# Kernel tuning notes

Measured on AMD Instinct MI355X. Metric: run time of the kernel, lower is better.

The kernel has to match this reference:

```python
import jax, jax.numpy as jnp
import numpy as np
import math

B, S, D, NPOS = 8, 2048, 768, 512


def setup_inputs() -> dict:
    key = jax.random.key(0)
    ks = jax.random.split(key, 9)
    std = 0.02
    return {
        "token_embeddings": jax.random.normal(ks[0], (B, S, D), dtype=jnp.float32),
        "attention_mask": jnp.ones((B, S), dtype=jnp.int32),
        "Wq": jax.random.normal(ks[1], (D, D), dtype=jnp.float32) * std,
        "bq": jax.random.normal(ks[2], (D,), dtype=jnp.float32) * std,
        "Wk": jax.random.normal(ks[3], (D, D), dtype=jnp.float32) * std,
        "bk": jax.random.normal(ks[4], (D,), dtype=jnp.float32) * std,
        "Wv": jax.random.normal(ks[5], (D, D), dtype=jnp.float32) * std,
        "bv": jax.random.normal(ks[6], (D,), dtype=jnp.float32) * std,
        "pos_emb": jax.random.normal(ks[7], (D, NPOS), dtype=jnp.float32) * std,
    }


def reference(token_embeddings, attention_mask, Wq, bq, Wk, bk, Wv, bv, pos_emb):
    scale = 1.0 / math.sqrt(D)
    q = token_embeddings @ Wq.T + bq  # [B,S,D]
    k = token_embeddings @ Wk.T + bk
    v = token_embeddings @ Wv.T + bv

    logits = jnp.einsum("bsd,btd->bst", q, k) * scale  # [B,S,S]
    logits = jnp.where(attention_mask[:, None, :] == 0, -jnp.inf, logits)

    # CoPE: gate-based fractional positions + interpolated learned bias
    gates = jax.nn.sigmoid(logits)
    pos = jnp.flip(jnp.cumsum(jnp.flip(gates, -1), axis=-1), -1)  # reverse cumsum
    pos = jnp.minimum(pos, float(NPOS - 1))
    pos_floor = jnp.floor(pos)
    pos_ceil = jnp.ceil(pos)
    logits_int = jnp.einsum("bsd,dn->bsn", q, pos_emb)  # [B,S,NPOS]
    lc = jnp.take_along_axis(logits_int, pos_ceil.astype(jnp.int32), axis=-1)
    lf = jnp.take_along_axis(logits_int, pos_floor.astype(jnp.int32), axis=-1)
    w = pos - pos_floor
    logits = logits + lc * w + lf * (1.0 - w)

    attn = jax.nn.softmax(logits, axis=-1)
    out = jnp.einsum("bst,btd->bsd", attn, v)
    return out[:, 0, :]  # CLS pooled sentence embedding [B,D]
```

## Files before the change

### kernel.cpp

```cpp
#include <hip/hip_runtime.h>
#include <hip/hip_bf16.h>
#include <math.h>

#define BB 8
#define SS 2048
#define DD 768
#define NPOS 512
#define TC 64
#define DSPLIT 16
#define DCHUNK (DD / DSPLIT)
#define ETOT 1280
#define SCALE 0.036084391824351615f

#define WS_Q      0
#define WS_QK     6144
#define WS_LI     12288
#define WS_LOGITS 16384
#define WS_ATTN   32768
#define WS_CTX    49152
#define WS_PART   55296
#define WS_PWS    448512

__device__ __forceinline__ float wave_reduce_sum(float v) {
    #pragma unroll
    for (int off = 32; off > 0; off >>= 1) v += __shfl_xor(v, off, 64);
    return v;
}

__global__ __launch_bounds__(256) void k_gemv(const float* __restrict__ vecs, size_t vstride,
        const float* __restrict__ W, const float* __restrict__ bias,
        float* __restrict__ out) {
    int gw = (blockIdx.x * 256 + threadIdx.x) >> 6;
    int lane = threadIdx.x & 63;
    if (gw >= BB * DD) return;
    int b = gw / DD, d = gw % DD;
    const float4* vr = (const float4*)(vecs + (size_t)b * vstride);
    const float4* wr = (const float4*)(W + (size_t)d * DD);
    float acc = 0.f;
    #pragma unroll
    for (int j = 0; j < 3; ++j) {
        float4 a = vr[lane + 64 * j];
        float4 w = wr[lane + 64 * j];
        acc += a.x * w.x + a.y * w.y + a.z * w.z + a.w * w.w;
    }
    acc = wave_reduce_sum(acc);
    if (lane == 0) out[gw] = acc + bias[d];
}

__global__ __launch_bounds__(256) void k_qkw(const float* __restrict__ q,
        const float* __restrict__ Wk, const float* __restrict__ pos_emb,
        float* __restrict__ pws) {
    int part = blockIdx.x, ds = blockIdx.y, tid = threadIdx.x;
    __shared__ float qs[BB][DCHUNK];
    for (int i = tid; i < BB * DCHUNK; i += 256) {
        int b = i / DCHUNK, d = i % DCHUNK;
        qs[b][d] = q[b * DD + ds * DCHUNK + d];
    }
    __syncthreads();
    const float* Wsrc; int stride, eg;
    if (part < 3) { Wsrc = Wk; stride = DD; eg = part * 256 + tid; }
    else { Wsrc = pos_emb; stride = NPOS; eg = DD + (part - 3) * 256 + tid; }
    int e = (part < 3) ? eg : eg - DD;
    const float* col = Wsrc + (size_t)(ds * DCHUNK) * stride + e;
    float acc[BB];
    #pragma unroll
    for (int b = 0; b < BB; ++b) acc[b] = 0.f;
    #pragma unroll
    for (int d = 0; d < DCHUNK; ++d) {
        float w = col[(size_t)d * stride];
        #pragma unroll
        for (int b = 0; b < BB; ++b) acc[b] += qs[b][d] * w;
    }
    #pragma unroll
    for (int b = 0; b < BB; ++b)
        pws[((size_t)ds * BB + b) * ETOT + eg] = acc[b];
}

__global__ __launch_bounds__(256) void k_qkr(const float* __restrict__ pws,
        float* __restrict__ qk, float* __restrict__ lint) {
    int idx = blockIdx.x * 256 + threadIdx.x;
    if (idx >= BB * ETOT) return;
    int b = idx / ETOT, e = idx % ETOT;
    float acc = 0.f;
    #pragma unroll
    for (int ds = 0; ds < DSPLIT; ++ds)
        acc += pws[((size_t)ds * BB + b) * ETOT + e];
    if (e < DD) qk[b * DD + e] = acc;
    else lint[b * NPOS + (e - DD)] = acc;
}

__global__ __launch_bounds__(256) void k_logits(const float* __restrict__ x,
        const float* __restrict__ qk, const float* __restrict__ q,
        const float* __restrict__ bk,
        const int* __restrict__ mask, float* __restrict__ logits) {
    int gw = (blockIdx.x * 256 + threadIdx.x) >> 6;
    int lane = threadIdx.x & 63;
    if (gw >= BB * SS) return;
    int b = gw / SS;
    const float4* xr = (const float4*)(x + (size_t)gw * DD);
    const float4* wr = (const float4*)(qk + (size_t)b * DD);
    const float4* qr = (const float4*)(q + (size_t)b * DD);
    const float4* br = (const float4*)bk;
    float acc = 0.f;
    #pragma unroll
    for (int j = 0; j < 3; ++j) {
        float4 a = xr[lane + 64 * j];
        float4 w = wr[lane + 64 * j];
        acc += a.x * w.x + a.y * w.y + a.z * w.z + a.w * w.w;
        float4 qv = qr[lane + 64 * j];
        float4 bv = br[lane + 64 * j];
        acc += qv.x * bv.x + qv.y * bv.y + qv.z * bv.z + qv.w * bv.w;
    }
    acc = wave_reduce_sum(acc);
    if (lane == 0) {
        float lg = acc * SCALE;
        logits[gw] = mask[gw] ? lg : -INFINITY;
    }
}

__global__ __launch_bounds__(256) void k_scan(const float* __restrict__ logits,
        const float* __restrict__ lint, float* __restrict__ attn) {
    int b = blockIdx.x, tid = threadIdx.x;
    __shared__ float lg[SS];
    __shared__ float li[NPOS];
    __shared__ float sa[256], sb[256];
    for (int i = tid; i < SS; i += 256) lg[i] = logits[b * SS + i];
    for (int i = tid; i < NPOS; i += 256) li[i] = lint[b * NPOS + i];
    __syncthreads();
    int base = tid * 8;
    float loc[8];
    float run = 0.f;
    #pragma unroll
    for (int k = 7; k >= 0; --k) {
        float v = lg[base + k];
        float gk = 1.f / (1.f + expf(-v));
        run += gk;
        loc[k] = run;
    }
    sa[tid] = run;
    __syncthreads();
    float* src = sa; float* dst = sb;
    for (int off = 1; off < 256; off <<= 1) {
        float v = src[tid];
        if (tid + off < 256) v += src[tid + off];
        dst[tid] = v;
        __syncthreads();
        float* t_ = src; src = dst; dst = t_;
    }
    float st = (tid < 255) ? src[tid + 1] : 0.f;
    float adj[8];
    float m = -INFINITY;
    #pragma unroll
    for (int k = 0; k < 8; ++k) {
        float v = lg[base + k];
        float nv;
        if (v == -INFINITY) {
            nv = v;
        } else {
            float p = fminf(loc[k] + st, (float)(NPOS - 1));
            float pf = floorf(p);
            float w = p - pf;
            int fi = (int)pf;
            int ci = (int)ceilf(p);
            nv = v + li[ci] * w + li[fi] * (1.f - w);
        }
        adj[k] = nv;
        m = fmaxf(m, nv);
    }
    __syncthreads();
    sa[tid] = m;
    __syncthreads();
    for (int s2 = 128; s2 > 0; s2 >>= 1) {
        if (tid < s2) sa[tid] = fmaxf(sa[tid], sa[tid + s2]);
        __syncthreads();
    }
    float bm = sa[0];
    __syncthreads();
    float sum = 0.f;
    #pragma unroll
    for (int k = 0; k < 8; ++k) { adj[k] = expf(adj[k] - bm); sum += adj[k]; }
    sa[tid] = sum;
    __syncthreads();
    for (int s2 = 128; s2 > 0; s2 >>= 1) {
        if (tid < s2) sa[tid] += sa[tid + s2];
        __syncthreads();
    }
    float inv = 1.f / sa[0];
    float4* out4 = (float4*)(attn + b * SS + base);
    out4[0] = make_float4(adj[0] * inv, adj[1] * inv, adj[2] * inv, adj[3] * inv);
    out4[1] = make_float4(adj[4] * inv, adj[5] * inv, adj[6] * inv, adj[7] * inv);
}

__global__ __launch_bounds__(192) void k_ctx_part(const float* __restrict__ x,
        const float* __restrict__ attn, float* __restrict__ part) {
    int tc = blockIdx.x, b = blockIdx.y, tid = threadIdx.x;
    const int TPC = SS / TC;
    float4 acc = make_float4(0.f, 0.f, 0.f, 0.f);
    const float4* xr = (const float4*)(x + ((size_t)b * SS + (size_t)tc * TPC) * DD);
    const float* at = attn + b * SS + tc * TPC;
    for (int i = 0; i < TPC; ++i) {
        float a = at[i];
        float4 xv = xr[(size_t)i * 192 + tid];
        acc.x += a * xv.x; acc.y += a * xv.y; acc.z += a * xv.z; acc.w += a * xv.w;
    }
    ((float4*)(part + (size_t)(b * TC + tc) * DD))[tid] = acc;
}

__global__ __launch_bounds__(256) void k_ctx_red(const float* __restrict__ part,
        float* __restrict__ ctx) {
    int idx = blockIdx.x * 256 + threadIdx.x;
    if (idx >= BB * DD) return;
    int b = idx / DD, e = idx % DD;
    float acc = 0.f;
    #pragma unroll 4
    for (int tc = 0; tc < TC; ++tc) acc += part[(size_t)(b * TC + tc) * DD + e];
    ctx[idx] = acc;
}

extern "C" void kernel_launch(void* const* d_in, const int* in_sizes, int n_in,
                              void* d_out, int out_size, void* d_ws, size_t ws_size,
                              hipStream_t stream) {
    const float* x       = (const float*)d_in[0];
    const int*   mask    = (const int*)  d_in[1];
    const float* Wq      = (const float*)d_in[2];
    const float* bq      = (const float*)d_in[3];
    const float* Wk      = (const float*)d_in[4];
    const float* bk      = (const float*)d_in[5];
    const float* Wv      = (const float*)d_in[6];
    const float* bv      = (const float*)d_in[7];
    const float* pos_emb = (const float*)d_in[8];
    float* out = (float*)d_out;

    float* ws     = (float*)d_ws;
    float* q      = ws + WS_Q;
    float* qk     = ws + WS_QK;
    float* lint   = ws + WS_LI;
    float* logits = ws + WS_LOGITS;
    float* attn   = ws + WS_ATTN;
    float* ctx    = ws + WS_CTX;
    float* part   = ws + WS_PART;
    float* pws    = ws + WS_PWS;

    k_gemv<<<dim3((BB * DD) / 4), dim3(256), 0, stream>>>(x, (size_t)SS * DD, Wq, bq, q);
    k_qkw<<<dim3(5, DSPLIT), dim3(256), 0, stream>>>(q, Wk, pos_emb, pws);
    k_qkr<<<dim3((BB * ETOT + 255) / 256), dim3(256), 0, stream>>>(pws, qk, lint);
    k_logits<<<dim3((BB * SS) / 4), dim3(256), 0, stream>>>(x, qk, q, bk, mask, logits);
    k_scan<<<dim3(BB), dim3(256), 0, stream>>>(logits, lint, attn);
    k_ctx_part<<<dim3(TC, BB), dim3(192), 0, stream>>>(x, attn, part);
    k_ctx_red<<<dim3((BB * DD + 255) / 256), dim3(256), 0, stream>>>(part, ctx);
    k_gemv<<<dim3((BB * DD) / 4), dim3(256), 0, stream>>>(ctx, (size_t)DD, Wv, bv, out);
}
```

Baseline: 49.80 us.

## Replace split-reduction kernels with atomics and use wave shuffles in scan

Removes the two separate reduction kernels (for q·Wk/pos_emb partials and the context partials) by accumulating with atomicAdd into zeroed buffers, cutting the launch count from eight to six. The zeroing is folded into the Q kernel and the scan kernel. The q·bk term is precomputed once per batch instead of being recomputed by every logit wave. The scan kernel's suffix sum, max and sum reductions now use wave shuffles with far fewer barriers. Atomics make the floating-point summation order nondeterministic, and DSPLIT doubles, which raises atomic traffic.

New measurement: 46.38 us. 6.9% less time.

```diff
diff --git a/kernel.cpp b/kernel.cpp
--- a/kernel.cpp
+++ b/kernel.cpp
@@ -7,35 +7,40 @@
 #define DD 768
 #define NPOS 512
 #define TC 64
-#define DSPLIT 16
+#define DSPLIT 32
 #define DCHUNK (DD / DSPLIT)
-#define ETOT 1280
 #define SCALE 0.036084391824351615f
 
 #define WS_Q      0
 #define WS_QK     6144
 #define WS_LI     12288
-#define WS_LOGITS 16384
-#define WS_ATTN   32768
-#define WS_CTX    49152
-#define WS_PART   55296
-#define WS_PWS    448512
-
-__device__ __forceinline__ float wave_reduce_sum(float v) {
+#define WS_QBK    16384
+#define WS_LOGITS 16400
+#define WS_ATTN   32784
+#define WS_CTX    49168
+
+__device__ __forceinline__ float wave_sum(float v) {
     #pragma unroll
     for (int off = 32; off > 0; off >>= 1) v += __shfl_xor(v, off, 64);
     return v;
 }
-
-__global__ __launch_bounds__(256) void k_gemv(const float* __restrict__ vecs, size_t vstride,
-        const float* __restrict__ W, const float* __restrict__ bias,
-        float* __restrict__ out) {
-    int gw = (blockIdx.x * 256 + threadIdx.x) >> 6;
+__device__ __forceinline__ float wave_max(float v) {
+    #pragma unroll
+    for (int off = 32; off > 0; off >>= 1) v = fmaxf(v, __shfl_xor(v, off, 64));
+    return v;
+}
+
+__global__ __launch_bounds__(256) void k_q(const float* __restrict__ x,
+        const float* __restrict__ Wq, const float* __restrict__ bq,
+        float* __restrict__ q, float* __restrict__ qkz) {
+    int zi = blockIdx.x * 256 + threadIdx.x;
+    if (zi < DD * BB + NPOS * BB) qkz[zi] = 0.f;
+    int gw = zi >> 6;
     int lane = threadIdx.x & 63;
     if (gw >= BB * DD) return;
     int b = gw / DD, d = gw % DD;
-    const float4* vr = (const float4*)(vecs + (size_t)b * vstride);
-    const float4* wr = (const float4*)(W + (size_t)d * DD);
+    const float4* vr = (const float4*)(x + (size_t)b * SS * DD);
+    const float4* wr = (const float4*)(Wq + (size_t)d * DD);
     float acc = 0.f;
     #pragma unroll
     for (int j = 0; j < 3; ++j) {
@@ -43,13 +48,14 @@
         float4 w = wr[lane + 64 * j];
         acc += a.x * w.x + a.y * w.y + a.z * w.z + a.w * w.w;
     }
-    acc = wave_reduce_sum(acc);
-    if (lane == 0) out[gw] = acc + bias[d];
+    acc = wave_sum(acc);
+    if (lane == 0) q[gw] = acc + bq[d];
 }
 
 __global__ __launch_bounds__(256) void k_qkw(const float* __restrict__ q,
         const float* __restrict__ Wk, const float* __restrict__ pos_emb,
-        float* __restrict__ pws) {
+        const float* __restrict__ bk,
+        float* __restrict__ qk, float* __restrict__ lint, float* __restrict__ qbk) {
     int part = blockIdx.x, ds = blockIdx.y, tid = threadIdx.x;
     __shared__ float qs[BB][DCHUNK];
     for (int i = tid; i < BB * DCHUNK; i += 256) {
@@ -57,10 +63,10 @@
         qs[b][d] = q[b * DD + ds * DCHUNK + d];
     }
     __syncthreads();
-    const float* Wsrc; int stride, eg;
-    if (part < 3) { Wsrc = Wk; stride = DD; eg = part * 256 + tid; }
-    else { Wsrc = pos_emb; stride = NPOS; eg = DD + (part - 3) * 256 + tid; }
-    int e = (part < 3) ? eg : eg - DD;
+    const float* Wsrc; int stride; float* dst; int e;
+    if (part < 3) { Wsrc = Wk; stride = DD; dst = qk; e = part * 256 + tid; }
+    else { Wsrc = pos_emb; stride = NPOS; dst = lint; e = (part - 3) * 256 + tid; }
+    int ncols = (part < 3) ? DD : NPOS;
     const float* col = Wsrc + (size_t)(ds * DCHUNK) * stride + e;
     float acc[BB];
     #pragma unroll
@@ -72,26 +78,24 @@
         for (int b = 0; b < BB; ++b) acc[b] += qs[b][d] * w;
     }
     #pragma unroll
-    for (int b = 0; b < BB; ++b)
-        pws[((size_t)ds * BB + b) * ETOT + eg] = acc[b];
-}
-
-__global__ __launch_bounds__(256) void k_qkr(const float* __restrict__ pws,
-        float* __restrict__ qk, float* __restrict__ lint) {
-    int idx = blockIdx.x * 256 + threadIdx.x;
-    if (idx >= BB * ETOT) return;
-    int b = idx / ETOT, e = idx % ETOT;
-    float acc = 0.f;
-    #pragma unroll
-    for (int ds = 0; ds < DSPLIT; ++ds)
-        acc += pws[((size_t)ds * BB + b) * ETOT + e];
-    if (e < DD) qk[b * DD + e] = acc;
-    else lint[b * NPOS + (e - DD)] = acc;
+    for (int b = 0; b < BB; ++b) atomicAdd(&dst[b * ncols + e], acc[b]);
+    if (part == 0 && ds == 0) {
+        int w = tid >> 6, lane = tid & 63;
+        #pragma unroll
+        for (int r = 0; r < 2; ++r) {
+            int b = w + 4 * r;
+            float p = 0.f;
+            #pragma unroll
+            for (int j = 0; j < 12; ++j)
+                p += q[b * DD + lane + 64 * j] * bk[lane + 64 * j];
+            p = wave_sum(p);
+            if (lane == 0) qbk[b] = p;
+        }
+    }
 }
 
 __global__ __launch_bounds__(256) void k_logits(const float* __restrict__ x,
-        const float* __restrict__ qk, const float* __restrict__ q,
-        const float* __restrict__ bk,
+        const float* __restrict__ qk, const float* __restrict__ qbk,
         const int* __restrict__ mask, float* __restrict__ logits) {
     int gw = (blockIdx.x * 256 + threadIdx.x) >> 6;
     int lane = threadIdx.x & 63;
@@ -99,100 +103,91 @@
     int b = gw / SS;
     const float4* xr = (const float4*)(x + (size_t)gw * DD);
     const float4* wr = (const float4*)(qk + (size_t)b * DD);
-    const float4* qr = (const float4*)(q + (size_t)b * DD);
-    const float4* br = (const float4*)bk;
     float acc = 0.f;
     #pragma unroll
     for (int j = 0; j < 3; ++j) {
         float4 a = xr[lane + 64 * j];
         float4 w = wr[lane + 64 * j];
         acc += a.x * w.x + a.y * w.y + a.z * w.z + a.w * w.w;
-        float4 qv = qr[lane + 64 * j];
-        float4 bv = br[lane + 64 * j];
-        acc += qv.x * bv.x + qv.y * bv.y + qv.z * bv.z + qv.w * bv.w;
-    }
-    acc = wave_reduce_sum(acc);
+    }
+    acc = wave_sum(acc);
     if (lane == 0) {
-        float lg = acc * SCALE;
+        float lg = (acc + qbk[b]) * SCALE;
         logits[gw] = mask[gw] ? lg : -INFINITY;
     }
 }
 
 __global__ __launch_bounds__(256) void k_scan(const float* __restrict__ logits,
-        const float* __restrict__ lint, float* __restrict__ attn) {
+        const float* __restrict__ lint, float* __restrict__ attn,
+        float* __restrict__ ctx) {
     int b = blockIdx.x, tid = threadIdx.x;
-    __shared__ float lg[SS];
+    int w = tid >> 6, lane = tid & 63;
     __shared__ float li[NPOS];
-    __shared__ float sa[256], sb[256];
-    for (int i = tid; i < SS; i += 256) lg[i] = logits[b * SS + i];
+    __shared__ float swt[4], smax[4], ssum[4];
+    #pragma unroll
+    for (int j = 0; j < 3; ++j) ctx[b * DD + tid + 256 * j] = 0.f;
     for (int i = tid; i < NPOS; i += 256) li[i] = lint[b * NPOS + i];
-    __syncthreads();
     int base = tid * 8;
+    const float4* lg4 = (const float4*)(logits + b * SS + base);
+    float4 l0 = lg4[0], l1 = lg4[1];
+    float lg[8] = {l0.x, l0.y, l0.z, l0.w, l1.x, l1.y, l1.z, l1.w};
     float loc[8];
     float run = 0.f;
     #pragma unroll
     for (int k = 7; k >= 0; --k) {
-        float v = lg[base + k];
-        float gk = 1.f / (1.f + expf(-v));
+        float gk = 1.f / (1.f + expf(-lg[k]));
         run += gk;
         loc[k] = run;
     }
-    sa[tid] = run;
-    __syncthreads();
-    float* src = sa; float* dst = sb;
-    for (int off = 1; off < 256; off <<= 1) {
-        float v = src[tid];
-        if (tid + off < 256) v += src[tid + off];
-        dst[tid] = v;
-        __syncthreads();
-        float* t_ = src; src = dst; dst = t_;
-    }
-    float st = (tid < 255) ? src[tid + 1] : 0.f;
+    float v = run;
+    #pragma unroll
+    for (int off = 1; off < 64; off <<= 1) {
+        float o = __shfl_down(v, off, 64);
+        if (lane + off < 64) v += o;
+    }
+    float sufExcl = (lane < 63) ? __shfl_down(v, 1, 64) : 0.f;
+    if (lane == 0) swt[w] = v;
+    __syncthreads();
+    float wsuf = 0.f;
+    for (int ww = w + 1; ww < 4; ++ww) wsuf += swt[ww];
+    float st = sufExcl + wsuf;
     float adj[8];
     float m = -INFINITY;
     #pragma unroll
     for (int k = 0; k < 8; ++k) {
-        float v = lg[base + k];
+        float val = lg[k];
         float nv;
-        if (v == -INFINITY) {
-            nv = v;
+        if (val == -INFINITY) {
+            nv = val;
         } else {
             float p = fminf(loc[k] + st, (float)(NPOS - 1));
             float pf = floorf(p);
-            float w = p - pf;
+            float wt = p - pf;
             int fi = (int)pf;
             int ci = (int)ceilf(p);
-            nv = v + li[ci] * w + li[fi] * (1.f - w);
+            nv = val + li[ci] * wt + li[fi] * (1.f - wt);
         }
         adj[k] = nv;
         m = fmaxf(m, nv);
     }
-    __syncthreads();
-    sa[tid] = m;
-    __syncthreads();
-    for (int s2 = 128; s2 > 0; s2 >>= 1) {
-        if (tid < s2) sa[tid] = fmaxf(sa[tid], sa[tid + s2]);
-        __syncthreads();
-    }
-    float bm = sa[0];
-    __syncthreads();
+    m = wave_max(m);
+    if (lane == 0) smax[w] = m;
+    __syncthreads();
+    float bm = fmaxf(fmaxf(smax[0], smax[1]), fmaxf(smax[2], smax[3]));
     float sum = 0.f;
     #pragma unroll
     for (int k = 0; k < 8; ++k) { adj[k] = expf(adj[k] - bm); sum += adj[k]; }
-    sa[tid] = sum;
-    __syncthreads();
-    for (int s2 = 128; s2 > 0; s2 >>= 1) {
-        if (tid < s2) sa[tid] += sa[tid + s2];
-        __syncthreads();
-    }
-    float inv = 1.f / sa[0];
+    sum = wave_sum(sum);
+    if (lane == 0) ssum[w] = sum;
+    __syncthreads();
+    float inv = 1.f / (ssum[0] + ssum[1] + ssum[2] + ssum[3]);
     float4* out4 = (float4*)(attn + b * SS + base);
     out4[0] = make_float4(adj[0] * inv, adj[1] * inv, adj[2] * inv, adj[3] * inv);
     out4[1] = make_float4(adj[4] * inv, adj[5] * inv, adj[6] * inv, adj[7] * inv);
 }
 
 __global__ __launch_bounds__(192) void k_ctx_part(const float* __restrict__ x,
-        const float* __restrict__ attn, float* __restrict__ part) {
+        const float* __restrict__ attn, float* __restrict__ ctx) {
     int tc = blockIdx.x, b = blockIdx.y, tid = threadIdx.x;
     const int TPC = SS / TC;
     float4 acc = make_float4(0.f, 0.f, 0.f, 0.f);
@@ -203,18 +198,31 @@
         float4 xv = xr[(size_t)i * 192 + tid];
         acc.x += a * xv.x; acc.y += a * xv.y; acc.z += a * xv.z; acc.w += a * xv.w;
     }
-    ((float4*)(part + (size_t)(b * TC + tc) * DD))[tid] = acc;
-}
-
-__global__ __launch_bounds__(256) void k_ctx_red(const float* __restrict__ part,
-        float* __restrict__ ctx) {
-    int idx = blockIdx.x * 256 + threadIdx.x;
-    if (idx >= BB * DD) return;
-    int b = idx / DD, e = idx % DD;
+    float* dst = ctx + b * DD + tid * 4;
+    atomicAdd(dst + 0, acc.x);
+    atomicAdd(dst + 1, acc.y);
+    atomicAdd(dst + 2, acc.z);
+    atomicAdd(dst + 3, acc.w);
+}
+
+__global__ __launch_bounds__(256) void k_out(const float* __restrict__ ctx,
+        const float* __restrict__ Wv, const float* __restrict__ bv,
+        float* __restrict__ out) {
+    int gw = (blockIdx.x * 256 + threadIdx.x) >> 6;
+    int lane = threadIdx.x & 63;
+    if (gw >= BB * DD) return;
+    int b = gw / DD, d = gw % DD;
+    const float4* vr = (const float4*)(ctx + (size_t)b * DD);
+    const float4* wr = (const float4*)(Wv + (size_t)d * DD);
     float acc = 0.f;
-    #pragma unroll 4
-    for (int tc = 0; tc < TC; ++tc) acc += part[(size_t)(b * TC + tc) * DD + e];
-    ctx[idx] = acc;
+    #pragma unroll
+    for (int j = 0; j < 3; ++j) {
+        float4 a = vr[lane + 64 * j];
+        float4 w = wr[lane + 64 * j];
+        acc += a.x * w.x + a.y * w.y + a.z * w.z + a.w * w.w;
+    }
+    acc = wave_sum(acc);
+    if (lane == 0) out[gw] = acc + bv[d];
 }
 
 extern "C" void kernel_launch(void* const* d_in, const int* in_sizes, int n_in,
@@ -235,18 +243,15 @@
     float* q      = ws + WS_Q;
     float* qk     = ws + WS_QK;
     float* lint   = ws + WS_LI;
+    float* qbk    = ws + WS_QBK;
     float* logits = ws + WS_LOGITS;
     float* attn   = ws + WS_ATTN;
     float* ctx    = ws + WS_CTX;
-    float* part   = ws + WS_PART;
-    float* pws    = ws + WS_PWS;
-
-    k_gemv<<<dim3((BB * DD) / 4), dim3(256), 0, stream>>>(x, (size_t)SS * DD, Wq, bq, q);
-    k_qkw<<<dim3(5, DSPLIT), dim3(256), 0, stream>>>(q, Wk, pos_emb, pws);
-    k_qkr<<<dim3((BB * ETOT + 255) / 256), dim3(256), 0, stream>>>(pws, qk, lint);
-    k_logits<<<dim3((BB * SS) / 4), dim3(256), 0, stream>>>(x, qk, q, bk, mask, logits);
-    k_scan<<<dim3(BB), dim3(256), 0, stream>>>(logits, lint, attn);
-    k_ctx_part<<<dim3(TC, BB), dim3(192), 0, stream>>>(x, attn, part);
-    k_ctx_red<<<dim3((BB * DD + 255) / 256), dim3(256), 0, stream>>>(part, ctx);
-    k_gemv<<<dim3((BB * DD) / 4), dim3(256), 0, stream>>>(ctx, (size_t)DD, Wv, bv, out);
-}
+
+    k_q<<<dim3((BB * DD) / 4), dim3(256), 0, stream>>>(x, Wq, bq, q, qk);
+    k_qkw<<<dim3(5, DSPLIT), dim3(256), 0, stream>>>(q, Wk, pos_emb, bk, qk, lint, qbk);
+    k_logits<<<dim3((BB * SS) / 4), dim3(256), 0, stream>>>(x, qk, qbk, mask, logits);
+    k_scan<<<dim3(BB), dim3(256), 0, stream>>>(logits, lint, attn, ctx);
+    k_ctx_part<<<dim3(TC, BB), dim3(192), 0, stream>>>(x, attn, ctx);
+    k_out<<<dim3((BB * DD) / 4), dim3(256), 0, stream>>>(ctx, Wv, bv, out);
+}
```

## Fuse prep stages into cooperative kernel and merge scan with context accumulation

Applied to the files above, without the earlier changes.

The first three stages (the q GEMV, the q·Wk and q·pos_emb products, and their split reduction) are merged into one cooperative kernel with grid-wide syncs. The q·bk dot product is computed once per batch instead of inside every logits wave. The softmax scan is fused into the context accumulation: each of 512 blocks recomputes the full per-batch scan and adds its partial into ctx with atomics, which removes the attention buffer and the separate reduction kernel. This cuts the launch count from 8 to 4, in exchange for redundant scan work, float atomic contention, and grid-sync overhead.

Result: slower. 105.5 us (+111.8%).

```diff
diff --git a/kernel.cpp b/kernel.cpp
--- a/kernel.cpp
+++ b/kernel.cpp
@@ -1,41 +1,245 @@
 #include <hip/hip_runtime.h>
-#include <hip/hip_bf16.h>
+#include <hip/hip_cooperative_groups.h>
 #include <math.h>
+
+namespace cg = cooperative_groups;
 
 #define BB 8
 #define SS 2048
 #define DD 768
 #define NPOS 512
 #define TC 64
-#define DSPLIT 16
+#define DSPLIT 32
 #define DCHUNK (DD / DSPLIT)
-#define ETOT 1280
+#define ETOT (DD + NPOS)
+#define PBLK (5 * DSPLIT)
 #define SCALE 0.036084391824351615f
 
 #define WS_Q      0
 #define WS_QK     6144
 #define WS_LI     12288
-#define WS_LOGITS 16384
-#define WS_ATTN   32768
-#define WS_CTX    49152
-#define WS_PART   55296
-#define WS_PWS    448512
-
-__device__ __forceinline__ float wave_reduce_sum(float v) {
+#define WS_QBK    16384
+#define WS_LOGITS 16400
+#define WS_CTX    32784
+#define WS_PWS    38928
+
+__device__ __forceinline__ float wave_sum(float v) {
     #pragma unroll
     for (int off = 32; off > 0; off >>= 1) v += __shfl_xor(v, off, 64);
     return v;
 }
 
-__global__ __launch_bounds__(256) void k_gemv(const float* __restrict__ vecs, size_t vstride,
-        const float* __restrict__ W, const float* __restrict__ bias,
+__global__ __launch_bounds__(256) void k_prep(
+        const float* __restrict__ x,
+        const float* __restrict__ Wq, const float* __restrict__ bq,
+        const float* __restrict__ Wk, const float* __restrict__ bk,
+        const float* __restrict__ pos_emb, float* __restrict__ ws) {
+    cg::grid_group grid = cg::this_grid();
+    const int tid  = threadIdx.x;
+    const int lane = tid & 63;
+    const int wid  = tid >> 6;
+    const int bid  = blockIdx.x;
+    const int gt   = bid * 256 + tid;
+
+    float* q    = ws + WS_Q;
+    float* qk   = ws + WS_QK;
+    float* lint = ws + WS_LI;
+    float* qbk  = ws + WS_QBK;
+    float* ctx  = ws + WS_CTX;
+    float* pws  = ws + WS_PWS;
+
+    __shared__ float qs[BB][DCHUNK];
+
+    if (gt < BB * DD) ctx[gt] = 0.f;
+    for (int o = bid * 4 + wid; o < BB * DD; o += PBLK * 4) {
+        int b = o / DD, d = o % DD;
+        const float4* vr = (const float4*)(x + (size_t)b * SS * DD);
+        const float4* wr = (const float4*)(Wq + (size_t)d * DD);
+        float acc = 0.f;
+        #pragma unroll
+        for (int j = 0; j < 3; ++j) {
+            float4 a = vr[lane + 64 * j];
+            float4 w = wr[lane + 64 * j];
+            acc += a.x * w.x + a.y * w.y + a.z * w.z + a.w * w.w;
+        }
+        acc = wave_sum(acc);
+        if (lane == 0) q[o] = acc + bq[d];
+    }
+    grid.sync();
+
+    {
+        int part = bid / DSPLIT;
+        int ds   = bid % DSPLIT;
+        for (int i = tid; i < BB * DCHUNK; i += 256) {
+            int b = i / DCHUNK, d = i % DCHUNK;
+            qs[b][d] = q[b * DD + ds * DCHUNK + d];
+        }
+        __syncthreads();
+        const float* Wsrc; int stride, eg;
+        if (part < 3) { Wsrc = Wk; stride = DD; eg = part * 256 + tid; }
+        else { Wsrc = pos_emb; stride = NPOS; eg = DD + (part - 3) * 256 + tid; }
+        int e = (part < 3) ? eg : eg - DD;
+        const float* col = Wsrc + (size_t)(ds * DCHUNK) * stride + e;
+        float acc[BB];
+        #pragma unroll
+        for (int b = 0; b < BB; ++b) acc[b] = 0.f;
+        #pragma unroll
+        for (int d = 0; d < DCHUNK; ++d) {
+            float w = col[(size_t)d * stride];
+            #pragma unroll
+            for (int b = 0; b < BB; ++b) acc[b] += qs[b][d] * w;
+        }
+        #pragma unroll
+        for (int b = 0; b < BB; ++b)
+            pws[((size_t)ds * BB + b) * ETOT + eg] = acc[b];
+        if (bid == 0) {
+            #pragma unroll
+            for (int r = 0; r < 2; ++r) {
+                int b = wid + 4 * r;
+                float p = 0.f;
+                #pragma unroll
+                for (int j = 0; j < 12; ++j)
+                    p += q[b * DD + lane + 64 * j] * bk[lane + 64 * j];
+                p = wave_sum(p);
+                if (lane == 0) qbk[b] = p;
+            }
+        }
+    }
+    grid.sync();
+
+    if (gt < BB * ETOT) {
+        int b = gt / ETOT, e = gt % ETOT;
+        float acc = 0.f;
+        #pragma unroll 4
+        for (int ds = 0; ds < DSPLIT; ++ds)
+            acc += pws[((size_t)ds * BB + b) * ETOT + e];
+        if (e < DD) qk[b * DD + e] = acc;
+        else lint[b * NPOS + (e - DD)] = acc;
+    }
+}
+
+__global__ __launch_bounds__(256) void k_logits(const float* __restrict__ x,
+        const float* __restrict__ qk, const float* __restrict__ qbk,
+        const int* __restrict__ mask, float* __restrict__ logits) {
+    int gw = (blockIdx.x * 256 + threadIdx.x) >> 6;
+    int lane = threadIdx.x & 63;
+    if (gw >= BB * SS) return;
+    int b = gw >> 11;
+    const float4* xr = (const float4*)(x + (size_t)gw * DD);
+    const float4* wr = (const float4*)(qk + (size_t)b * DD);
+    float acc = 0.f;
+    #pragma unroll
+    for (int j = 0; j < 3; ++j) {
+        float4 a = xr[lane + 64 * j];
+        float4 w = wr[lane + 64 * j];
+        acc += a.x * w.x + a.y * w.y + a.z * w.z + a.w * w.w;
+    }
+    acc = wave_sum(acc);
+    if (lane == 0) {
+        float lg = (acc + qbk[b]) * SCALE;
+        logits[gw] = mask[gw] ? lg : -INFINITY;
+    }
+}
+
+__global__ __launch_bounds__(256) void k_ctxscan(const float* __restrict__ x,
+        const float* __restrict__ logits, const float* __restrict__ lint,
+        float* __restrict__ ctx) {
+    int tc = blockIdx.x, b = blockIdx.y, tid = threadIdx.x;
+    __shared__ float lg[SS];
+    __shared__ float li[NPOS];
+    __shared__ float sa[256], sb[256];
+    for (int i = tid; i < SS; i += 256) lg[i] = logits[b * SS + i];
+    for (int i = tid; i < NPOS; i += 256) li[i] = lint[b * NPOS + i];
+    __syncthreads();
+    int base = tid * 8;
+    float loc[8];
+    float run = 0.f;
+    #pragma unroll
+    for (int k = 7; k >= 0; --k) {
+        float v = lg[base + k];
+        float gk = 1.f / (1.f + expf(-v));
+        run += gk;
+        loc[k] = run;
+    }
+    sa[tid] = run;
+    __syncthreads();
+    float* src = sa; float* dst = sb;
+    for (int off = 1; off < 256; off <<= 1) {
+        float v = src[tid];
+        if (tid + off < 256) v += src[tid + off];
+        dst[tid] = v;
+        __syncthreads();
+        float* t_ = src; src = dst; dst = t_;
+    }
+    float st = (tid < 255) ? src[tid + 1] : 0.f;
+    float adj[8];
+    float m = -INFINITY;
+    #pragma unroll
+    for (int k = 0; k < 8; ++k) {
+        float val = lg[base + k];
+        float nv;
+        if (val == -INFINITY) {
+            nv = val;
+        } else {
+            float p = fminf(loc[k] + st, (float)(NPOS - 1));
+            float pf = floorf(p);
+            float wt = p - pf;
+            int fi = (int)pf;
+            int ci = (int)ceilf(p);
+            nv = val + li[ci] * wt + li[fi] * (1.f - wt);
+        }
+        adj[k] = nv;
+        m = fmaxf(m, nv);
+    }
+    __syncthreads();
+    sa[tid] = m;
+    __syncthreads();
+    for (int s2 = 128; s2 > 0; s2 >>= 1) {
+        if (tid < s2) sa[tid] = fmaxf(sa[tid], sa[tid + s2]);
+        __syncthreads();
+    }
+    float bm = sa[0];
+    __syncthreads();
+    float sum = 0.f;
+    #pragma unroll
+    for (int k = 0; k < 8; ++k) { adj[k] = expf(adj[k] - bm); sum += adj[k]; }
+    sa[tid] = sum;
+    __syncthreads();
+    for (int s2 = 128; s2 > 0; s2 >>= 1) {
+        if (tid < s2) sa[tid] += sa[tid + s2];
+        __syncthreads();
+    }
+    float inv = 1.f / sa[0];
+    #pragma unroll
+    for (int k = 0; k < 8; ++k) lg[base + k] = adj[k] * inv;
+    __syncthreads();
+    if (tid < 192) {
+        const int TPC = SS / TC;
+        float4 acc = make_float4(0.f, 0.f, 0.f, 0.f);
+        const float4* xr = (const float4*)(x + ((size_t)b * SS + (size_t)tc * TPC) * DD);
+        const float* at = lg + tc * TPC;
+        for (int i = 0; i < TPC; ++i) {
+            float a = at[i];
+            float4 xv = xr[(size_t)i * 192 + tid];
+            acc.x += a * xv.x; acc.y += a * xv.y; acc.z += a * xv.z; acc.w += a * xv.w;
+        }
+        float* dstp = ctx + b * DD + tid * 4;
+        atomicAdd(dstp + 0, acc.x);
+        atomicAdd(dstp + 1, acc.y);
+        atomicAdd(dstp + 2, acc.z);
+        atomicAdd(dstp + 3, acc.w);
+    }
+}
+
+__global__ __launch_bounds__(256) void k_out(const float* __restrict__ ctx,
+        const float* __restrict__ Wv, const float* __restrict__ bv,
         float* __restrict__ out) {
     int gw = (blockIdx.x * 256 + threadIdx.x) >> 6;
     int lane = threadIdx.x & 63;
     if (gw >= BB * DD) return;
     int b = gw / DD, d = gw % DD;
-    const float4* vr = (const float4*)(vecs + (size_t)b * vstride);
-    const float4* wr = (const float4*)(W + (size_t)d * DD);
+    const float4* vr = (const float4*)(ctx + (size_t)b * DD);
+    const float4* wr = (const float4*)(Wv + (size_t)d * DD);
     float acc = 0.f;
     #pragma unroll
     for (int j = 0; j < 3; ++j) {
@@ -43,178 +247,8 @@
         float4 w = wr[lane + 64 * j];
         acc += a.x * w.x + a.y * w.y + a.z * w.z + a.w * w.w;
     }
-    acc = wave_reduce_sum(acc);
-    if (lane == 0) out[gw] = acc + bias[d];
-}
-
-__global__ __launch_bounds__(256) void k_qkw(const float* __restrict__ q,
-        const float* __restrict__ Wk, const float* __restrict__ pos_emb,
-        float* __restrict__ pws) {
-    int part = blockIdx.x, ds = blockIdx.y, tid = threadIdx.x;
-    __shared__ float qs[BB][DCHUNK];
-    for (int i = tid; i < BB * DCHUNK; i += 256) {
-        int b = i / DCHUNK, d = i % DCHUNK;
-        qs[b][d] = q[b * DD + ds * DCHUNK + d];
-    }
-    __syncthreads();
-    const float* Wsrc; int stride, eg;
-    if (part < 3) { Wsrc = Wk; stride = DD; eg = part * 256 + tid; }
-    else { Wsrc = pos_emb; stride = NPOS; eg = DD + (part - 3) * 256 + tid; }
-    int e = (part < 3) ? eg : eg - DD;
-    const float* col = Wsrc + (size_t)(ds * DCHUNK) * stride + e;
-    float acc[BB];
-    #pragma unroll
-    for (int b = 0; b < BB; ++b) acc[b] = 0.f;
-    #pragma unroll
-    for (int d = 0; d < DCHUNK; ++d) {
-        float w = col[(size_t)d * stride];
-        #pragma unroll
-        for (int b = 0; b < BB; ++b) acc[b] += qs[b][d] * w;
-    }
-    #pragma unroll
-    for (int b = 0; b < BB; ++b)
-        pws[((size_t)ds * BB + b) * ETOT + eg] = acc[b];
-}
-
-__global__ __launch_bounds__(256) void k_qkr(const float* __restrict__ pws,
-        float* __restrict__ qk, float* __restrict__ lint) {
-    int idx = blockIdx.x * 256 + threadIdx.x;
-    if (idx >= BB * ETOT) return;
-    int b = idx / ETOT, e = idx % ETOT;
-    float acc = 0.f;
-    #pragma unroll
-    for (int ds = 0; ds < DSPLIT; ++ds)
-        acc += pws[((size_t)ds * BB + b) * ETOT + e];
-    if (e < DD) qk[b * DD + e] = acc;
-    else lint[b * NPOS + (e - DD)] = acc;
-}
-
-__global__ __launch_bounds__(256) void k_logits(const float* __restrict__ x,
-        const float* __restrict__ qk, const float* __restrict__ q,
-        const float* __restrict__ bk,
-        const int* __restrict__ mask, float* __restrict__ logits) {
-    int gw = (blockIdx.x * 256 + threadIdx.x) >> 6;
-    int lane = threadIdx.x & 63;
-    if (gw >= BB * SS) return;
-    int b = gw / SS;
-    const float4* xr = (const float4*)(x + (size_t)gw * DD);
-    const float4* wr = (const float4*)(qk + (size_t)b * DD);
-    const float4* qr = (const float4*)(q + (size_t)b * DD);
-    const float4* br = (const float4*)bk;
-    float acc = 0.f;
-    #pragma unroll
-    for (int j = 0; j < 3; ++j) {
-        float4 a = xr[lane + 64 * j];
-        float4 w = wr[lane + 64 * j];
-        acc += a.x * w.x + a.y * w.y + a.z * w.z + a.w * w.w;
-        float4 qv = qr[lane + 64 * j];
-        float4 bv = br[lane + 64 * j];
-        acc += qv.x * bv.x + qv.y * bv.y + qv.z * bv.z + qv.w * bv.w;
-    }
-    acc = wave_reduce_sum(acc);
-    if (lane == 0) {
-        float lg = acc * SCALE;
-        logits[gw] = mask[gw] ? lg : -INFINITY;
-    }
-}
-
-__global__ __launch_bounds__(256) void k_scan(const float* __restrict__ logits,
-        const float* __restrict__ lint, float* __restrict__ attn) {
-    int b = blockIdx.x, tid = threadIdx.x;
-    __shared__ float lg[SS];
-    __shared__ float li[NPOS];
-    __shared__ float sa[256], sb[256];
-    for (int i = tid; i < SS; i += 256) lg[i] = logits[b * SS + i];
-    for (int i = tid; i < NPOS; i += 256) li[i] = lint[b * NPOS + i];
-    __syncthreads();
-    int base = tid * 8;
-    float loc[8];
-    float run = 0.f;
-    #pragma unroll
-    for (int k = 7; k >= 0; --k) {
-        float v = lg[base + k];
-        float gk = 1.f / (1.f + expf(-v));
-        run += gk;
-        loc[k] = run;
-    }
-    sa[tid] = run;
-    __syncthreads();
-    float* src = sa; float* dst = sb;
-    for (int off = 1; off < 256; off <<= 1) {
-        float v = src[tid];
-        if (tid + off < 256) v += src[tid + off];
-        dst[tid] = v;
-        __syncthreads();
-        float* t_ = src; src = dst; dst = t_;
-    }
-    float st = (tid < 255) ? src[tid + 1] : 0.f;
-    float adj[8];
-    float m = -INFINITY;
-    #pragma unroll
-    for (int k = 0; k < 8; ++k) {
-        float v = lg[base + k];
-        float nv;
-        if (v == -INFINITY) {
-            nv = v;
-        } else {
-            float p = fminf(loc[k] + st, (float)(NPOS - 1));
-            float pf = floorf(p);
-            float w = p - pf;
-            int fi = (int)pf;
-            int ci = (int)ceilf(p);
-            nv = v + li[ci] * w + li[fi] * (1.f - w);
-        }
-        adj[k] = nv;
-        m = fmaxf(m, nv);
-    }
-    __syncthreads();
-    sa[tid] = m;
-    __syncthreads();
-    for (int s2 = 128; s2 > 0; s2 >>= 1) {
-        if (tid < s2) sa[tid] = fmaxf(sa[tid], sa[tid + s2]);
-        __syncthreads();
-    }
-    float bm = sa[0];
-    __syncthreads();
-    float sum = 0.f;
-    #pragma unroll
-    for (int k = 0; k < 8; ++k) { adj[k] = expf(adj[k] - bm); sum += adj[k]; }
-    sa[tid] = sum;
-    __syncthreads();
-    for (int s2 = 128; s2 > 0; s2 >>= 1) {
-        if (tid < s2) sa[tid] += sa[tid + s2];
-        __syncthreads();
-    }
-    float inv = 1.f / sa[0];
-    float4* out4 = (float4*)(attn + b * SS + base);
-    out4[0] = make_float4(adj[0] * inv, adj[1] * inv, adj[2] * inv, adj[3] * inv);
-    out4[1] = make_float4(adj[4] * inv, adj[5] * inv, adj[6] * inv, adj[7] * inv);
-}
-
-__global__ __launch_bounds__(192) void k_ctx_part(const float* __restrict__ x,
-        const float* __restrict__ attn, float* __restrict__ part) {
-    int tc = blockIdx.x, b = blockIdx.y, tid = threadIdx.x;
-    const int TPC = SS / TC;
-    float4 acc = make_float4(0.f, 0.f, 0.f, 0.f);
-    const float4* xr = (const float4*)(x + ((size_t)b * SS + (size_t)tc * TPC) * DD);
-    const float* at = attn + b * SS + tc * TPC;
-    for (int i = 0; i < TPC; ++i) {
-        float a = at[i];
-        float4 xv = xr[(size_t)i * 192 + tid];
-        acc.x += a * xv.x; acc.y += a * xv.y; acc.z += a * xv.z; acc.w += a * xv.w;
-    }
-    ((float4*)(part + (size_t)(b * TC + tc) * DD))[tid] = acc;
-}
-
-__global__ __launch_bounds__(256) void k_ctx_red(const float* __restrict__ part,
-        float* __restrict__ ctx) {
-    int idx = blockIdx.x * 256 + threadIdx.x;
-    if (idx >= BB * DD) return;
-    int b = idx / DD, e = idx % DD;
-    float acc = 0.f;
-    #pragma unroll 4
-    for (int tc = 0; tc < TC; ++tc) acc += part[(size_t)(b * TC + tc) * DD + e];
-    ctx[idx] = acc;
+    acc = wave_sum(acc);
+    if (lane == 0) out[gw] = acc + bv[d];
 }
 
 extern "C" void kernel_launch(void* const* d_in, const int* in_sizes, int n_in,
@@ -230,23 +264,19 @@
     const float* bv      = (const float*)d_in[7];
     const float* pos_emb = (const float*)d_in[8];
     float* out = (float*)d_out;
-
-    float* ws     = (float*)d_ws;
+    float* ws  = (float*)d_ws;
+
     float* q      = ws + WS_Q;
     float* qk     = ws + WS_QK;
     float* lint   = ws + WS_LI;
+    float* qbk    = ws + WS_QBK;
     float* logits = ws + WS_LOGITS;
-    float* attn   = ws + WS_ATTN;
     float* ctx    = ws + WS_CTX;
-    float* part   = ws + WS_PART;
-    float* pws    = ws + WS_PWS;
-
-    k_gemv<<<dim3((BB * DD) / 4), dim3(256), 0, stream>>>(x, (size_t)SS * DD, Wq, bq, q);
-    k_qkw<<<dim3(5, DSPLIT), dim3(256), 0, stream>>>(q, Wk, pos_emb, pws);
-    k_qkr<<<dim3((BB * ETOT + 255) / 256), dim3(256), 0, stream>>>(pws, qk, lint);
-    k_logits<<<dim3((BB * SS) / 4), dim3(256), 0, stream>>>(x, qk, q, bk, mask, logits);
-    k_scan<<<dim3(BB), dim3(256), 0, stream>>>(logits, lint, attn);
-    k_ctx_part<<<dim3(TC, BB), dim3(192), 0, stream>>>(x, attn, part);
-    k_ctx_red<<<dim3((BB * DD + 255) / 256), dim3(256), 0, stream>>>(part, ctx);
-    k_gemv<<<dim3((BB * DD) / 4), dim3(256), 0, stream>>>(ctx, (size_t)DD, Wv, bv, out);
-}
+
+    void* args[] = {(void*)&x, (void*)&Wq, (void*)&bq, (void*)&Wk,
+                    (void*)&bk, (void*)&pos_emb, (void*)&ws};
+    hipLaunchCooperativeKernel((void*)k_prep, dim3(PBLK), dim3(256), args, 0, stream);
+    k_logits<<<dim3((BB * SS) / 4), dim3(256), 0, stream>>>(x, qk, qbk, mask, logits);
+    k_ctxscan<<<dim3(TC, BB), dim3(256), 0, stream>>>(x, logits, lint, ctx);
+    k_out<<<dim3((BB * DD) / 4), dim3(256), 0, stream>>>(ctx, Wv, bv, out);
+}
```
